# Kernel optimization log

Measured on AMD Instinct MI355X. Metric: run time of the kernel, lower is better.

## Reference

```python
import jax, jax.numpy as jnp
import numpy as np

B, N, C_IN, FC0, K = 16, 32768, 32, 256, 1024
CHUNK = 64  # chunk over the K=1024 attention channels to bound the [N,CHUNK,C] intermediate
BN_EPS = 1e-5


def _lengths():
    rng = np.random.default_rng(0)
    r = rng.integers(1024, 3072, size=B)
    l = (r * N) // r.sum()
    l[-1] += N - l.sum()
    assert l.min() > 0 and l.sum() == N
    return jnp.asarray(l, dtype=jnp.int32)


def setup_inputs() -> dict:
    key = jax.random.key(0)
    ks = jax.random.split(key, 16)
    f32 = jnp.float32
    x = jax.random.normal(ks[0], (N, C_IN), dtype=f32)
    # conv1d_1 (1x1 conv == per-point linear), BN1
    w1 = jax.random.normal(ks[1], (FC0, C_IN), dtype=f32) * 0.1
    b1 = jax.random.normal(ks[2], (FC0,), dtype=f32) * 0.1
    g1 = 1.0 + 0.1 * jax.random.normal(ks[3], (FC0,), dtype=f32)
    be1 = 0.1 * jax.random.normal(ks[4], (FC0,), dtype=f32)
    m1 = 0.1 * jax.random.normal(ks[5], (FC0,), dtype=f32)
    v1 = 0.5 + jax.random.uniform(ks[6], (FC0,), dtype=f32)
    # conv1d_2, BN2
    w2 = jax.random.normal(ks[7], (K, FC0), dtype=f32) * 0.05
    b2 = jax.random.normal(ks[8], (K,), dtype=f32) * 0.1
    g2 = 1.0 + 0.1 * jax.random.normal(ks[9], (K,), dtype=f32)
    be2 = 0.1 * jax.random.normal(ks[10], (K,), dtype=f32)
    m2 = 0.1 * jax.random.normal(ks[11], (K,), dtype=f32)
    v2 = 0.5 + jax.random.uniform(ks[12], (K,), dtype=f32)
    # fc_1, BN3
    fcw = jax.random.normal(ks[13], (FC0, C_IN * K), dtype=f32) * 0.01
    fcb = jax.random.normal(ks[14], (FC0,), dtype=f32) * 0.1
    kb = jax.random.split(ks[15], 4)
    g3 = 1.0 + 0.1 * jax.random.normal(kb[0], (FC0,), dtype=f32)
    be3 = 0.1 * jax.random.normal(kb[1], (FC0,), dtype=f32)
    m3 = 0.1 * jax.random.normal(kb[2], (FC0,), dtype=f32)
    v3 = 0.5 + jax.random.uniform(kb[3], (FC0,), dtype=f32)
    return dict(x=x, length=_lengths(), w1=w1, b1=b1, g1=g1, be1=be1, m1=m1, v1=v1,
                w2=w2, b2=b2, g2=g2, be2=be2, m2=m2, v2=v2,
                fcw=fcw, fcb=fcb, g3=g3, be3=be3, m3=m3, v3=v3)


def _bn(x, g, b, m, v):
    # eval-mode BatchNorm (running stats)
    return (x - m) * (g * jax.lax.rsqrt(v + BN_EPS)) + b


def _forward(x, length, w1, b1, g1, be1, m1, v1, w2, b2, g2, be2, m2, v2,
             fcw, fcb, g3, be3, m3, v3):
    # attention features: conv1x1 -> BN -> ReLU, twice  -> [N, K]
    att = jax.nn.relu(_bn(x @ w1.T + b1, g1, be1, m1, v1))
    att = jax.nn.relu(_bn(att @ w2.T + b2, g2, be2, m2, v2))

    seg = jnp.repeat(jnp.arange(B, dtype=jnp.int32), length, total_repeat_length=N)  # [N]

    # per-segment softmax over the point axis (torch F.softmax(..., dim=0))
    mx = jax.ops.segment_max(att, seg, num_segments=B)              # [B, K]
    e = jnp.exp(att - mx[seg])
    w = e / jax.ops.segment_sum(e, seg, num_segments=B)[seg]        # [N, K]

    # per-segment weighted pooling: out[b] = att_b.T @ x_b, chunked over K
    chunks = []
    for s in range(0, K, CHUNK):
        contrib = w[:, s:s + CHUNK, None] * x[:, None, :]           # [N, CHUNK, C]
        chunks.append(jax.ops.segment_sum(contrib, seg, num_segments=B))
    pooled = jnp.concatenate(chunks, axis=1)                        # [B, K, C]
    pooled = pooled / length[:, None, None].astype(x.dtype)
    out2 = pooled.reshape(B, K * C_IN)                              # row-major flatten of [K, C]

    r = _bn(out2 @ fcw.T + fcb, g3, be3, m3, v3)                    # [B, 256]
    # F.normalize(p=2, dim=1, eps=1e-12)
    return r / jnp.maximum(jnp.linalg.norm(r, axis=1, keepdims=True), 1e-12)


def reference(x, length, w1, b1, g1, be1, m1, v1, w2, b2, g2, be2, m2, v2,
              fcw, fcb, g3, be3, m3, v3):
    return _forward(x, length, w1, b1, g1, be1, m1, v1, w2, b2, g2, be2, m2, v2,
                    fcw, fcb, g3, be3, m3, v3)
```

## Files before the change

kernel.cpp:

```cpp
#include <hip/hip_runtime.h>
#include <hip/hip_bf16.h>

typedef __bf16 bf16x8 __attribute__((ext_vector_type(8)));
typedef unsigned short u16x4 __attribute__((ext_vector_type(4)));
typedef unsigned short u16x8 __attribute__((ext_vector_type(8)));
typedef float f32x4 __attribute__((ext_vector_type(4)));
typedef unsigned long long ull;

__device__ inline unsigned short f2bf(float f) {
    unsigned u = __builtin_bit_cast(unsigned, f);
    unsigned r = (u + 0x7fffu + ((u >> 16) & 1u)) >> 16;
    return (unsigned short)r;
}
__device__ inline float bf2f(unsigned short h) {
    unsigned u = ((unsigned)h) << 16;
    return __builtin_bit_cast(float, u);
}

__device__ inline void gload_lds16(const void* g, void* l) {
    __builtin_amdgcn_global_load_lds((const __attribute__((address_space(1))) void*)g,
                                     (__attribute__((address_space(3))) void*)l, 16, 0, 0);
}

#define MAXCH 272

__global__ __launch_bounds__(256) void k01_prep_gemm1(const float* __restrict__ x,
                                                      const float* __restrict__ w1,
                                                      const float* __restrict__ b1,
                                                      const float* __restrict__ g1,
                                                      const float* __restrict__ be1,
                                                      const float* __restrict__ m1,
                                                      const float* __restrict__ v1,
                                                      const float* __restrict__ w2,
                                                      const int* __restrict__ length,
                                                      unsigned short* __restrict__ w2p,
                                                      int* __restrict__ meta,
                                                      unsigned short* __restrict__ att1) {
    __shared__ __align__(16) unsigned short st[64 * 256];
    int tid = threadIdx.x;
    int i = blockIdx.x * 256 + tid;
    if (i < 32768) {
        int kb = i >> 9, kk = (i >> 6) & 7, l = i & 63;
        int col = kb * 16 + (l & 15);
        int kin = kk * 32 + (l >> 4) * 8;
        unsigned short v[8];
#pragma unroll
        for (int j = 0; j < 8; j++) v[j] = f2bf(w2[(size_t)col * 256 + kin + j]);
        *(ull*)(w2p + (size_t)i * 8)     = *(ull*)&v[0];
        *(ull*)(w2p + (size_t)i * 8 + 4) = *(ull*)&v[4];
    }
    if (blockIdx.x == 0 && tid < 64) {
        int lane = tid;
        int b = lane & 15;
        int len = length[b];
        int off = 0, chbase = 0, nch = 0;
        int nchb = (len + 127) >> 7;
#pragma unroll
        for (int j = 0; j < 16; j++) {
            int lj = __shfl(len, j, 64);
            int nj = __shfl(nchb, j, 64);
            if (j < b) { off += lj; chbase += nj; }
            nch += nj;
        }
        int total = __shfl(off + len, 15, 64);
        if (lane < 16) {
            meta[b] = off;
            meta[848 + b] = chbase;
            meta[864 + b] = chbase + nchb;
            if (b == 0) { meta[16] = total; meta[17] = nch; }
            for (int t = 0; t < nchb; t++) {
                int s = off + t * 128;
                int en = off + len < s + 128 ? off + len : s + 128;
                meta[304 + chbase + t] = s;
                meta[576 + chbase + t] = en;
            }
        }
    }
    int row0 = blockIdx.x * 64;
    int lane = tid & 63, wave = tid >> 6;
    int lr = lane & 15, s16 = lane >> 4;

    bf16x8 a[4], b[4];
#pragma unroll
    for (int m = 0; m < 4; m++) {
        const float* xp = x + (size_t)(row0 + m * 16 + lr) * 32 + s16 * 8;
        f32x4 lo = *(const f32x4*)(const void*)xp;
        f32x4 hi = *(const f32x4*)(const void*)(xp + 4);
        unsigned short v[8];
#pragma unroll
        for (int j = 0; j < 4; j++) { v[j] = f2bf(lo[j]); v[4 + j] = f2bf(hi[j]); }
        a[m] = *(bf16x8*)v;
    }
#pragma unroll
    for (int n = 0; n < 4; n++) {
        const float* wp = w1 + (size_t)(wave * 64 + n * 16 + lr) * 32 + s16 * 8;
        f32x4 lo = *(const f32x4*)(const void*)wp;
        f32x4 hi = *(const f32x4*)(const void*)(wp + 4);
        unsigned short v[8];
#pragma unroll
        for (int j = 0; j < 4; j++) { v[j] = f2bf(lo[j]); v[4 + j] = f2bf(hi[j]); }
        b[n] = *(bf16x8*)v;
    }
    f32x4 acc[4][4] = {};
#pragma unroll
    for (int m = 0; m < 4; m++)
#pragma unroll
        for (int n = 0; n < 4; n++)
            acc[m][n] = __builtin_amdgcn_mfma_f32_16x16x32_bf16(a[m], b[n], acc[m][n], 0, 0, 0);

    int cc = lane & 15, cr4 = (lane >> 4) * 4;
#pragma unroll
    for (int n = 0; n < 4; n++) {
        int j = wave * 64 + n * 16 + cc;
        float s = g1[j] * rsqrtf(v1[j] + 1e-5f);
        float bias = (b1[j] - m1[j]) * s + be1[j];
#pragma unroll
        for (int m = 0; m < 4; m++) {
#pragma unroll
            for (int rg = 0; rg < 4; rg++) {
                int rl = m * 16 + cr4 + rg;
                float t = fmaf(acc[m][n][rg], s, bias);
                st[rl * 256 + j] = f2bf(fmaxf(t, 0.f));
            }
        }
    }
    __syncthreads();
#pragma unroll
    for (int p = 0; p < 8; p++) {
        int idx = p * 256 + tid;
        *(f32x4*)(void*)(att1 + (size_t)row0 * 256 + idx * 8) =
            *(const f32x4*)(const void*)((const char*)st + idx * 16);
    }
}

__global__ __launch_bounds__(256, 2) void k23_fused(const unsigned short* __restrict__ att1,
                                                    const unsigned short* __restrict__ w2p,
                                                    const float* __restrict__ x,
                                                    const int* __restrict__ meta,
                                                    const float* __restrict__ b2,
                                                    const float* __restrict__ g2,
                                                    const float* __restrict__ be2,
                                                    const float* __restrict__ m2,
                                                    const float* __restrict__ v2,
                                                    unsigned short* __restrict__ pP,
                                                    float* __restrict__ pS) {
    __shared__ __align__(16) unsigned short As[2][128 * 64];
    __shared__ __align__(16) unsigned short xT[48 * 128];
    int flat = blockIdx.x;
    int xcd = flat & 7, q = flat >> 3;
    int ch = (q >> 3) * 8 + xcd;
    int kt = q & 7;
    if (ch >= meta[17]) return;
    int n0 = meta[304 + ch];
    int rows = meta[576 + ch] - n0;
    int col0 = kt * 128;
    int tid = threadIdx.x, lane = tid & 63, wave = tid >> 6;
    int lr = lane & 15, s16 = lane >> 4;
    int wr = wave >> 1, wc = wave & 1;

    auto stage = [&](int t, int buf) {
#pragma unroll
        for (int it = 0; it < 4; it++) {
            int idx = it * 256 + tid;
            int row = idx >> 3, slot = idx & 7;
            int srow = row < rows ? row : rows - 1;
            int g = slot ^ (row & 7);
            gload_lds16(att1 + (size_t)(n0 + srow) * 256 + t * 64 + g * 8,
                        (char*)As + buf * 16384 + it * 4096 + wave * 1024);
        }
    };

    int kb0 = kt * 8 + wc * 4;
    auto loadB = [&](int t, bf16x8 (&bb)[2][4]) {
#pragma unroll
        for (int kk = 0; kk < 2; kk++)
#pragma unroll
            for (int n = 0; n < 4; n++)
                bb[kk][n] = *(const bf16x8*)(const void*)(
                    w2p + (size_t)(((kb0 + n) * 8 + t * 2 + kk) * 64 + lane) * 8);
    };

    bf16x8 b0[2][4], b1[2][4];
    stage(0, 0);
    loadB(0, b0);

#pragma unroll
    for (int p = 0; p < 8; p++) {
        int nb = p * 16 + (tid >> 5) * 2;
        int c = tid & 31;
        float v0 = (nb < rows) ? x[(size_t)(n0 + nb) * 32 + c] : 0.f;
        float v1 = (nb + 1 < rows) ? x[(size_t)(n0 + nb + 1) * 32 + c] : 0.f;
        unsigned pk = ((unsigned)f2bf(v1) << 16) | f2bf(v0);
        int byte = c * 256 + ((nb * 2) ^ ((c & 15) << 4));
        *(unsigned*)((char*)xT + byte) = pk;
    }
    if (tid < 128) {
        int byte = 32 * 256 + tid * 2;
        *(unsigned short*)((char*)xT + byte) = (tid < rows) ? f2bf(1.f) : (unsigned short)0;
    }
    __syncthreads();

    f32x4 acc[4][4] = {};
#pragma unroll
    for (int t = 0; t < 4; t++) {
        if (t < 3) stage(t + 1, (t & 1) ^ 1);
        if (t == 0) loadB(1, b1);
        else if (t == 1) loadB(2, b0);
        else if (t == 2) loadB(3, b1);
        const char* Ab = (const char*)As + (t & 1) * 16384;
#pragma unroll
        for (int kk = 0; kk < 2; kk++) {
            bf16x8 a[4];
#pragma unroll
            for (int m = 0; m < 4; m++) {
                int row = wr * 64 + m * 16 + lr;
                int slot = (kk * 4 + s16) ^ (row & 7);
                a[m] = *(const bf16x8*)(const void*)(Ab + row * 128 + slot * 16);
            }
#pragma unroll
            for (int m = 0; m < 4; m++)
#pragma unroll
                for (int n = 0; n < 4; n++)
                    acc[m][n] = __builtin_amdgcn_mfma_f32_16x16x32_bf16(
                        a[m], (t & 1) ? b1[kk][n] : b0[kk][n], acc[m][n], 0, 0, 0);
        }
        __syncthreads();
    }

    char* eT = (char*)As;
#pragma unroll
    for (int nf = 0; nf < 4; nf++) {
        int k = wc * 64 + nf * 16 + lr;
        int kg = col0 + k;
        float sc = g2[kg] * rsqrtf(v2[kg] + 1e-5f);
        float bias = (b2[kg] - m2[kg]) * sc + be2[kg];
#pragma unroll
        for (int m = 0; m < 4; m++) {
            int nbase = wr * 64 + m * 16 + s16 * 4;
            ull pk = 0;
#pragma unroll
            for (int rg = 0; rg < 4; rg++) {
                float tt = fmaf(acc[m][nf][rg], sc, bias);
                float ev = __expf(fmaxf(tt, 0.f));
                unsigned short h = (nbase + rg < rows) ? f2bf(ev) : (unsigned short)0;
                pk |= ((ull)h) << (16 * rg);
            }
            int byte = k * 256 + ((nbase * 2) ^ ((k & 15) << 4));
            *(ull*)(eT + byte) = pk;
        }
    }
    __syncthreads();

    f32x4 pacc[2][3] = {};
#pragma unroll
    for (int nc = 0; nc < 128; nc += 32) {
        bf16x8 ea[2], xb[3];
#pragma unroll
        for (int i = 0; i < 2; i++) {
            int k = (wave * 2 + i) * 16 + lr;
            int byte = k * 256 + (((nc + s16 * 8) * 2) ^ ((k & 15) << 4));
            ea[i] = *(const bf16x8*)(const void*)(eT + byte);
        }
#pragma unroll
        for (int j = 0; j < 3; j++) {
            int c = j * 16 + lr;
            int byte = c * 256 + (((nc + s16 * 8) * 2) ^ ((c & 15) << 4));
            xb[j] = *(const bf16x8*)(const void*)((const char*)xT + byte);
        }
#pragma unroll
        for (int i = 0; i < 2; i++)
#pragma unroll
            for (int j = 0; j < 3; j++)
                pacc[i][j] = __builtin_amdgcn_mfma_f32_16x16x32_bf16(ea[i], xb[j], pacc[i][j], 0, 0, 0);
    }

    unsigned short* pPc = pP + (size_t)ch * 32768;
#pragma unroll
    for (int i = 0; i < 2; i++) {
#pragma unroll
        for (int j = 0; j < 3; j++) {
            int c = j * 16 + lr;
#pragma unroll
            for (int rg = 0; rg < 4; rg++) {
                int k = (wave * 2 + i) * 16 + s16 * 4 + rg;
                float v = pacc[i][j][rg];
                if (c < 32) pPc[(col0 + k) * 32 + c] = f2bf(v);
                else if (c == 32) pS[ch * 1024 + col0 + k] = v;
            }
        }
    }
}

__global__ __launch_bounds__(256) void k3b_reduce(const unsigned short* __restrict__ pP,
                                                  const float* __restrict__ pS,
                                                  const int* __restrict__ meta,
                                                  float* __restrict__ out2) {
    int id = blockIdx.x * 256 + threadIdx.x;
    int base = id * 4;
    int b = base >> 15, rem = base & 32767, k = rem >> 5;
    float P[4] = {};
    float S = 0.f;
    int c0 = meta[848 + b], c1 = meta[864 + b];
    for (int ch = c0; ch < c1; ch++) {
        u16x4 v = *(const u16x4*)(const void*)(pP + (size_t)ch * 32768 + rem);
#pragma unroll
        for (int j = 0; j < 4; j++) P[j] += bf2f(v[j]);
        S += pS[ch * 1024 + k];
    }
    float inv = 1.f / (S * (float)(meta[b + 1] - meta[b]));
    f32x4 o = {P[0] * inv, P[1] * inv, P[2] * inv, P[3] * inv};
    *(f32x4*)(void*)(out2 + base) = o;
}

__global__ __launch_bounds__(256) void k4_fc(const float* __restrict__ out2,
                                             const float* __restrict__ fcw,
                                             float* __restrict__ pFC) {
    int jt = blockIdx.x, dc = blockIdx.y;
    int tid = threadIdx.x;
    float acc[16][8] = {};
#pragma unroll
    for (int i = 0; i < 8; i++) {
        int d = dc * 2048 + i * 256 + tid;
        float wv[8];
#pragma unroll
        for (int jj = 0; jj < 8; jj++) wv[jj] = fcw[(size_t)(jt * 8 + jj) * 32768 + d];
#pragma unroll
        for (int bb = 0; bb < 16; bb++) {
            float ov = out2[bb * 32768 + d];
#pragma unroll
            for (int jj = 0; jj < 8; jj++) acc[bb][jj] = fmaf(ov, wv[jj], acc[bb][jj]);
        }
    }
    __shared__ float red[32][257];
#pragma unroll
    for (int p = 0; p < 4; p++) {
#pragma unroll
        for (int q = 0; q < 4; q++)
#pragma unroll
            for (int jj = 0; jj < 8; jj++)
                red[q * 8 + jj][tid] = acc[p * 4 + q][jj];
        __syncthreads();
        int row = tid >> 3, sg = tid & 7;
        float s = 0.f;
        for (int u = sg; u < 256; u += 8) s += red[row][u];
        s += __shfl_down(s, 4, 8);
        s += __shfl_down(s, 2, 8);
        s += __shfl_down(s, 1, 8);
        if (sg == 0) {
            int bb = p * 4 + (row >> 3), jj = row & 7;
            pFC[(dc * 16 + bb) * 256 + jt * 8 + jj] = s;
        }
        __syncthreads();
    }
}

__global__ __launch_bounds__(256) void k45_fc2(const float* __restrict__ pFC,
                                               const float* __restrict__ fcb,
                                               const float* __restrict__ g3,
                                               const float* __restrict__ be3,
                                               const float* __restrict__ m3,
                                               const float* __restrict__ v3,
                                               float* __restrict__ out) {
    int b = blockIdx.x, j = threadIdx.x;
    float sum = 0.f;
#pragma unroll
    for (int dc = 0; dc < 16; dc++) sum += pFC[(dc * 16 + b) * 256 + j];
    float sc = g3[j] * rsqrtf(v3[j] + 1e-5f);
    float rv = (sum + fcb[j] - m3[j]) * sc + be3[j];
    float sq = rv * rv;
#pragma unroll
    for (int o = 32; o > 0; o >>= 1) sq += __shfl_down(sq, o, 64);
    __shared__ float wsum[4];
    if ((j & 63) == 0) wsum[j >> 6] = sq;
    __syncthreads();
    float tot = wsum[0] + wsum[1] + wsum[2] + wsum[3];
    out[b * 256 + j] = rv / fmaxf(sqrtf(tot), 1e-12f);
}

extern "C" void kernel_launch(void* const* d_in, const int* in_sizes, int n_in,
                              void* d_out, int out_size, void* d_ws, size_t ws_size,
                              hipStream_t stream) {
    const float* x    = (const float*)d_in[0];
    const int*   len  = (const int*)d_in[1];
    const float* w1   = (const float*)d_in[2];
    const float* b1   = (const float*)d_in[3];
    const float* g1   = (const float*)d_in[4];
    const float* be1  = (const float*)d_in[5];
    const float* m1   = (const float*)d_in[6];
    const float* v1   = (const float*)d_in[7];
    const float* w2   = (const float*)d_in[8];
    const float* b2   = (const float*)d_in[9];
    const float* g2   = (const float*)d_in[10];
    const float* be2  = (const float*)d_in[11];
    const float* m2   = (const float*)d_in[12];
    const float* v2   = (const float*)d_in[13];
    const float* fcw  = (const float*)d_in[14];
    const float* fcb  = (const float*)d_in[15];
    const float* g3   = (const float*)d_in[16];
    const float* be3  = (const float*)d_in[17];
    const float* m3   = (const float*)d_in[18];
    const float* v3   = (const float*)d_in[19];

    char* ws = (char*)d_ws;
    int* meta            = (int*)ws;
    unsigned short* w2p  = (unsigned short*)(ws + 4096);
    unsigned short* att1 = (unsigned short*)(ws + 528384);
    unsigned short* pP   = (unsigned short*)(ws + 17305600);
    float* pS            = (float*)(ws + 35131392);
    float* out2          = (float*)(ws + 36245504);
    float* pFC           = (float*)(ws + 38342656);
    float* out           = (float*)d_out;

    hipLaunchKernelGGL(k01_prep_gemm1, dim3(512),   dim3(256), 0, stream,
                       x, w1, b1, g1, be1, m1, v1, w2, len, w2p, meta, att1);
    hipLaunchKernelGGL(k23_fused,  dim3(MAXCH * 8), dim3(256), 0, stream, att1, w2p, x, meta, b2, g2, be2, m2, v2, pP, pS);
    hipLaunchKernelGGL(k3b_reduce, dim3(512),       dim3(256), 0, stream, pP, pS, meta, out2);
    hipLaunchKernelGGL(k4_fc,      dim3(32, 16),    dim3(256), 0, stream, out2, fcw, pFC);
    hipLaunchKernelGGL(k45_fc2,    dim3(16),        dim3(256), 0, stream, pFC, fcb, g3, be3, m3, v3, out);
}
```

Baseline: 78.86 us.

## Fuse first pointwise GEMM into second GEMM kernel, recompute per K-tile

Drops the att1 global intermediate. Each k123 block now recomputes the first 1x1-conv GEMM (x@w1, BN, ReLU) for its 128-row chunk straight into a full 128x256 swizzled LDS tile, then runs the second GEMM from LDS. This removes the 16MB bf16 write and re-read of att1 and the double-buffered global->LDS staging, and w1 is pre-packed to bf16 in the prep kernel. The cost is that the cheap GEMM1 is recomputed 8 times, once per K-tile block, and LDS per block grows to 64KB plus xT, which may limit occupancy at launch_bounds(256,2).

```diff
diff --git a/kernel.cpp b/kernel.cpp
--- a/kernel.cpp
+++ b/kernel.cpp
@@ -3,7 +3,6 @@
 
 typedef __bf16 bf16x8 __attribute__((ext_vector_type(8)));
 typedef unsigned short u16x4 __attribute__((ext_vector_type(4)));
-typedef unsigned short u16x8 __attribute__((ext_vector_type(8)));
 typedef float f32x4 __attribute__((ext_vector_type(4)));
 typedef unsigned long long ull;
 
@@ -17,26 +16,14 @@
     return __builtin_bit_cast(float, u);
 }
 
-__device__ inline void gload_lds16(const void* g, void* l) {
-    __builtin_amdgcn_global_load_lds((const __attribute__((address_space(1))) void*)g,
-                                     (__attribute__((address_space(3))) void*)l, 16, 0, 0);
-}
-
 #define MAXCH 272
 
-__global__ __launch_bounds__(256) void k01_prep_gemm1(const float* __restrict__ x,
-                                                      const float* __restrict__ w1,
-                                                      const float* __restrict__ b1,
-                                                      const float* __restrict__ g1,
-                                                      const float* __restrict__ be1,
-                                                      const float* __restrict__ m1,
-                                                      const float* __restrict__ v1,
-                                                      const float* __restrict__ w2,
-                                                      const int* __restrict__ length,
-                                                      unsigned short* __restrict__ w2p,
-                                                      int* __restrict__ meta,
-                                                      unsigned short* __restrict__ att1) {
-    __shared__ __align__(16) unsigned short st[64 * 256];
+__global__ __launch_bounds__(256) void k0_prep(const float* __restrict__ w1,
+                                               const float* __restrict__ w2,
+                                               const int* __restrict__ length,
+                                               unsigned short* __restrict__ w2p,
+                                               unsigned short* __restrict__ w1p,
+                                               int* __restrict__ meta) {
     int tid = threadIdx.x;
     int i = blockIdx.x * 256 + tid;
     if (i < 32768) {
@@ -48,6 +35,16 @@
         for (int j = 0; j < 8; j++) v[j] = f2bf(w2[(size_t)col * 256 + kin + j]);
         *(ull*)(w2p + (size_t)i * 8)     = *(ull*)&v[0];
         *(ull*)(w2p + (size_t)i * 8 + 4) = *(ull*)&v[4];
+    } else if (i < 32768 + 1024) {
+        int s = i - 32768;
+        int cb = s >> 6, l = s & 63;
+        int col = cb * 16 + (l & 15);
+        int kin = (l >> 4) * 8;
+        unsigned short v[8];
+#pragma unroll
+        for (int j = 0; j < 8; j++) v[j] = f2bf(w1[(size_t)col * 32 + kin + j]);
+        *(ull*)(w1p + (size_t)s * 8)     = *(ull*)&v[0];
+        *(ull*)(w1p + (size_t)s * 8 + 4) = *(ull*)&v[4];
     }
     if (blockIdx.x == 0 && tid < 64) {
         int lane = tid;
@@ -76,75 +73,25 @@
             }
         }
     }
-    int row0 = blockIdx.x * 64;
-    int lane = tid & 63, wave = tid >> 6;
-    int lr = lane & 15, s16 = lane >> 4;
-
-    bf16x8 a[4], b[4];
-#pragma unroll
-    for (int m = 0; m < 4; m++) {
-        const float* xp = x + (size_t)(row0 + m * 16 + lr) * 32 + s16 * 8;
-        f32x4 lo = *(const f32x4*)(const void*)xp;
-        f32x4 hi = *(const f32x4*)(const void*)(xp + 4);
-        unsigned short v[8];
-#pragma unroll
-        for (int j = 0; j < 4; j++) { v[j] = f2bf(lo[j]); v[4 + j] = f2bf(hi[j]); }
-        a[m] = *(bf16x8*)v;
-    }
-#pragma unroll
-    for (int n = 0; n < 4; n++) {
-        const float* wp = w1 + (size_t)(wave * 64 + n * 16 + lr) * 32 + s16 * 8;
-        f32x4 lo = *(const f32x4*)(const void*)wp;
-        f32x4 hi = *(const f32x4*)(const void*)(wp + 4);
-        unsigned short v[8];
-#pragma unroll
-        for (int j = 0; j < 4; j++) { v[j] = f2bf(lo[j]); v[4 + j] = f2bf(hi[j]); }
-        b[n] = *(bf16x8*)v;
-    }
-    f32x4 acc[4][4] = {};
-#pragma unroll
-    for (int m = 0; m < 4; m++)
-#pragma unroll
-        for (int n = 0; n < 4; n++)
-            acc[m][n] = __builtin_amdgcn_mfma_f32_16x16x32_bf16(a[m], b[n], acc[m][n], 0, 0, 0);
-
-    int cc = lane & 15, cr4 = (lane >> 4) * 4;
-#pragma unroll
-    for (int n = 0; n < 4; n++) {
-        int j = wave * 64 + n * 16 + cc;
-        float s = g1[j] * rsqrtf(v1[j] + 1e-5f);
-        float bias = (b1[j] - m1[j]) * s + be1[j];
-#pragma unroll
-        for (int m = 0; m < 4; m++) {
-#pragma unroll
-            for (int rg = 0; rg < 4; rg++) {
-                int rl = m * 16 + cr4 + rg;
-                float t = fmaf(acc[m][n][rg], s, bias);
-                st[rl * 256 + j] = f2bf(fmaxf(t, 0.f));
-            }
-        }
-    }
-    __syncthreads();
-#pragma unroll
-    for (int p = 0; p < 8; p++) {
-        int idx = p * 256 + tid;
-        *(f32x4*)(void*)(att1 + (size_t)row0 * 256 + idx * 8) =
-            *(const f32x4*)(const void*)((const char*)st + idx * 16);
-    }
-}
-
-__global__ __launch_bounds__(256, 2) void k23_fused(const unsigned short* __restrict__ att1,
-                                                    const unsigned short* __restrict__ w2p,
-                                                    const float* __restrict__ x,
-                                                    const int* __restrict__ meta,
-                                                    const float* __restrict__ b2,
-                                                    const float* __restrict__ g2,
-                                                    const float* __restrict__ be2,
-                                                    const float* __restrict__ m2,
-                                                    const float* __restrict__ v2,
-                                                    unsigned short* __restrict__ pP,
-                                                    float* __restrict__ pS) {
-    __shared__ __align__(16) unsigned short As[2][128 * 64];
+}
+
+__global__ __launch_bounds__(256, 2) void k123_fused(const float* __restrict__ x,
+                                                     const unsigned short* __restrict__ w1p,
+                                                     const unsigned short* __restrict__ w2p,
+                                                     const int* __restrict__ meta,
+                                                     const float* __restrict__ b1,
+                                                     const float* __restrict__ g1,
+                                                     const float* __restrict__ be1,
+                                                     const float* __restrict__ m1,
+                                                     const float* __restrict__ v1,
+                                                     const float* __restrict__ b2,
+                                                     const float* __restrict__ g2,
+                                                     const float* __restrict__ be2,
+                                                     const float* __restrict__ m2,
+                                                     const float* __restrict__ v2,
+                                                     unsigned short* __restrict__ pP,
+                                                     float* __restrict__ pS) {
+    __shared__ __align__(16) unsigned short As[128 * 256];
     __shared__ __align__(16) unsigned short xT[48 * 128];
     int flat = blockIdx.x;
     int xcd = flat & 7, q = flat >> 3;
@@ -153,36 +100,55 @@
     if (ch >= meta[17]) return;
     int n0 = meta[304 + ch];
     int rows = meta[576 + ch] - n0;
+    int N = meta[16];
     int col0 = kt * 128;
     int tid = threadIdx.x, lane = tid & 63, wave = tid >> 6;
     int lr = lane & 15, s16 = lane >> 4;
     int wr = wave >> 1, wc = wave & 1;
 
-    auto stage = [&](int t, int buf) {
-#pragma unroll
-        for (int it = 0; it < 4; it++) {
-            int idx = it * 256 + tid;
-            int row = idx >> 3, slot = idx & 7;
-            int srow = row < rows ? row : rows - 1;
-            int g = slot ^ (row & 7);
-            gload_lds16(att1 + (size_t)(n0 + srow) * 256 + t * 64 + g * 8,
-                        (char*)As + buf * 16384 + it * 4096 + wave * 1024);
-        }
-    };
-
-    int kb0 = kt * 8 + wc * 4;
-    auto loadB = [&](int t, bf16x8 (&bb)[2][4]) {
-#pragma unroll
-        for (int kk = 0; kk < 2; kk++)
+    bf16x8 A1[2];
+#pragma unroll
+    for (int m = 0; m < 2; m++) {
+        int ra = n0 + wave * 32 + m * 16 + lr;
+        if (ra >= N) ra = N - 1;
+        const float* xp = x + (size_t)ra * 32 + s16 * 8;
+        f32x4 lo = *(const f32x4*)(const void*)xp;
+        f32x4 hi = *(const f32x4*)(const void*)(xp + 4);
+        unsigned short v[8];
+#pragma unroll
+        for (int j = 0; j < 4; j++) { v[j] = f2bf(lo[j]); v[4 + j] = f2bf(hi[j]); }
+        A1[m] = *(bf16x8*)v;
+    }
+    int cc = lane & 15, cr4 = (lane >> 4) * 4;
+#pragma unroll
+    for (int cb = 0; cb < 4; cb++) {
+        bf16x8 B1[4];
+#pragma unroll
+        for (int n = 0; n < 4; n++)
+            B1[n] = *(const bf16x8*)(const void*)(w1p + (size_t)((cb * 4 + n) * 64 + lane) * 8);
+        f32x4 acc1[2][4] = {};
+#pragma unroll
+        for (int m = 0; m < 2; m++)
 #pragma unroll
             for (int n = 0; n < 4; n++)
-                bb[kk][n] = *(const bf16x8*)(const void*)(
-                    w2p + (size_t)(((kb0 + n) * 8 + t * 2 + kk) * 64 + lane) * 8);
-    };
-
-    bf16x8 b0[2][4], b1[2][4];
-    stage(0, 0);
-    loadB(0, b0);
+                acc1[m][n] = __builtin_amdgcn_mfma_f32_16x16x32_bf16(A1[m], B1[n], acc1[m][n], 0, 0, 0);
+#pragma unroll
+        for (int n = 0; n < 4; n++) {
+            int j = cb * 64 + n * 16 + cc;
+            float s = g1[j] * rsqrtf(v1[j] + 1e-5f);
+            float bias = (b1[j] - m1[j]) * s + be1[j];
+#pragma unroll
+            for (int m = 0; m < 2; m++) {
+#pragma unroll
+                for (int rg = 0; rg < 4; rg++) {
+                    int row = wave * 32 + m * 16 + cr4 + rg;
+                    float t = fmaf(acc1[m][n][rg], s, bias);
+                    int byte = row * 512 + (((j >> 3) ^ (row & 31)) << 4) + (j & 7) * 2;
+                    *(unsigned short*)((char*)As + byte) = f2bf(fmaxf(t, 0.f));
+                }
+            }
+        }
+    }
 
 #pragma unroll
     for (int p = 0; p < 8; p++) {
@@ -201,31 +167,27 @@
     __syncthreads();
 
     f32x4 acc[4][4] = {};
-#pragma unroll
-    for (int t = 0; t < 4; t++) {
-        if (t < 3) stage(t + 1, (t & 1) ^ 1);
-        if (t == 0) loadB(1, b1);
-        else if (t == 1) loadB(2, b0);
-        else if (t == 2) loadB(3, b1);
-        const char* Ab = (const char*)As + (t & 1) * 16384;
-#pragma unroll
-        for (int kk = 0; kk < 2; kk++) {
-            bf16x8 a[4];
-#pragma unroll
-            for (int m = 0; m < 4; m++) {
-                int row = wr * 64 + m * 16 + lr;
-                int slot = (kk * 4 + s16) ^ (row & 7);
-                a[m] = *(const bf16x8*)(const void*)(Ab + row * 128 + slot * 16);
-            }
-#pragma unroll
-            for (int m = 0; m < 4; m++)
-#pragma unroll
-                for (int n = 0; n < 4; n++)
-                    acc[m][n] = __builtin_amdgcn_mfma_f32_16x16x32_bf16(
-                        a[m], (t & 1) ? b1[kk][n] : b0[kk][n], acc[m][n], 0, 0, 0);
-        }
-        __syncthreads();
-    }
+    int kb0 = kt * 8 + wc * 4;
+#pragma unroll
+    for (int kk = 0; kk < 8; kk++) {
+        bf16x8 a[4], b[4];
+#pragma unroll
+        for (int n = 0; n < 4; n++)
+            b[n] = *(const bf16x8*)(const void*)(
+                w2p + (size_t)(((kb0 + n) * 8 + kk) * 64 + lane) * 8);
+#pragma unroll
+        for (int m = 0; m < 4; m++) {
+            int row = wr * 64 + m * 16 + lr;
+            int ps = (kk * 4 + s16) ^ (row & 31);
+            a[m] = *(const bf16x8*)(const void*)((const char*)As + row * 512 + ps * 16);
+        }
+#pragma unroll
+        for (int m = 0; m < 4; m++)
+#pragma unroll
+            for (int n = 0; n < 4; n++)
+                acc[m][n] = __builtin_amdgcn_mfma_f32_16x16x32_bf16(a[m], b[n], acc[m][n], 0, 0, 0);
+    }
+    __syncthreads();
 
     char* eT = (char*)As;
 #pragma unroll
@@ -404,16 +366,16 @@
     char* ws = (char*)d_ws;
     int* meta            = (int*)ws;
     unsigned short* w2p  = (unsigned short*)(ws + 4096);
-    unsigned short* att1 = (unsigned short*)(ws + 528384);
-    unsigned short* pP   = (unsigned short*)(ws + 17305600);
-    float* pS            = (float*)(ws + 35131392);
-    float* out2          = (float*)(ws + 36245504);
-    float* pFC           = (float*)(ws + 38342656);
+    unsigned short* w1p  = (unsigned short*)(ws + 528384);
+    unsigned short* pP   = (unsigned short*)(ws + 544768);
+    float* pS            = (float*)(ws + 18370560);
+    float* out2          = (float*)(ws + 19484672);
+    float* pFC           = (float*)(ws + 21581824);
     float* out           = (float*)d_out;
 
-    hipLaunchKernelGGL(k01_prep_gemm1, dim3(512),   dim3(256), 0, stream,
-                       x, w1, b1, g1, be1, m1, v1, w2, len, w2p, meta, att1);
-    hipLaunchKernelGGL(k23_fused,  dim3(MAXCH * 8), dim3(256), 0, stream, att1, w2p, x, meta, b2, g2, be2, m2, v2, pP, pS);
+    hipLaunchKernelGGL(k0_prep,    dim3(132),       dim3(256), 0, stream, w1, w2, len, w2p, w1p, meta);
+    hipLaunchKernelGGL(k123_fused, dim3(MAXCH * 8), dim3(256), 0, stream,
+                       x, w1p, w2p, meta, b1, g1, be1, m1, v1, b2, g2, be2, m2, v2, pP, pS);
     hipLaunchKernelGGL(k3b_reduce, dim3(512),       dim3(256), 0, stream, pP, pS, meta, out2);
     hipLaunchKernelGGL(k4_fc,      dim3(32, 16),    dim3(256), 0, stream, out2, fcw, pFC);
     hipLaunchKernelGGL(k45_fc2,    dim3(16),        dim3(256), 0, stream, pFC, fcb, g3, be3, m3, v3, out);
```

After: 97.66 us. 1.24x slower.
